# Performance work log

Hardware: AMD Instinct MI355X
Metric: run time of the kernel (lower is better)

The kernel has to match this reference:

```python
import jax, jax.numpy as jnp
import numpy as np

N = 50000   # nodes
E = 400000  # edges
G = 256     # graphs in batch
D = 256     # out_dim (scalar channel width)
VD = 16     # vector channel width after v_emb


def setup_inputs() -> dict:
    key = jax.random.key(0)
    ks = jax.random.split(key, 12)

    def rn(k, shape, scale=0.02):
        return (jax.random.normal(k, shape) * scale).astype(jnp.float32)

    return dict(
        node_s=jax.random.normal(ks[0], (N, 23), jnp.float32),
        node_v=jax.random.normal(ks[1], (N, 4, 3), jnp.float32),
        edge_s=jax.random.normal(ks[2], (E, 17), jnp.float32),
        edge_index=jax.random.randint(ks[3], (2, E), 0, N, jnp.int32),
        batch=jnp.sort(jax.random.randint(ks[4], (N,), 0, G, jnp.int32)),
        Ws=rn(ks[5], (23, D)), bs=jnp.zeros((D,), jnp.float32),
        Wv=rn(ks[6], (4, VD)), bv=jnp.zeros((VD,), jnp.float32),
        We=rn(ks[7], (18, D)), be=jnp.zeros((D,), jnp.float32),
        Wm1=rn(ks[8], (2 * D + VD + D, D)), bm1=jnp.zeros((D,), jnp.float32),
        Wm2=rn(ks[9], (D, D)), bm2=jnp.zeros((D,), jnp.float32),
        Wn=rn(ks[10], (D + VD, D)), bn=jnp.zeros((D,), jnp.float32),
        gamma=jnp.ones((D,), jnp.float32), beta=jnp.zeros((D,), jnp.float32),
    )


def reference(node_s, node_v, edge_s, edge_index, batch,
              Ws, bs, Wv, bv, We, be, Wm1, bm1, Wm2, bm2, Wn, bn, gamma, beta):
    # --- embeddings ---
    s = node_s @ Ws + bs                                            # [N, D]
    e_in = jnp.concatenate([edge_s, jnp.zeros((edge_s.shape[0], 1), edge_s.dtype)], axis=-1)  # no edge_v branch
    e = e_in @ We + be                                              # [E, D]
    # v_emb: Linear over the 4 vector channels -> [N, VD, 3]
    v = jnp.einsum('nkc,ko->noc', node_v, Wv) + bv[None, :, None]
    v_norm = jnp.linalg.norm(v, axis=-1)                            # [N, VD]

    # --- SimpleGVPConv: gather -> 2-layer MLP per edge -> scatter-mean ---
    src, dst = edge_index[0], edge_index[1]                         # PyG: s_j = s[src], s_i = s[dst]
    m_in = jnp.concatenate([s[dst], s[src], v_norm[src], e], axis=-1)  # [E, 2D+VD+D]
    m = jax.nn.relu(m_in @ Wm1 + bm1) @ Wm2 + bm2                   # [E, D]
    agg = jax.ops.segment_sum(m, dst, num_segments=N)               # [N, D]
    cnt = jax.ops.segment_sum(jnp.ones((E,), m.dtype), dst, num_segments=N)
    s = s + agg / jnp.maximum(cnt, 1.0)[:, None]                    # mean aggr + residual update

    # --- node MLP: Linear -> LayerNorm -> ReLU (dropout = eval identity) ---
    feat = jnp.concatenate([s, v_norm], axis=-1)                    # [N, D+VD]
    h = feat @ Wn + bn                                              # [N, D]
    mu = h.mean(axis=-1, keepdims=True)
    var = h.var(axis=-1, keepdims=True)
    h = (h - mu) * jax.lax.rsqrt(var + 1e-5) * gamma + beta
    h = jax.nn.relu(h)

    # --- global mean pool ---
    gsum = jax.ops.segment_sum(h, batch, num_segments=G)            # [G, D]
    gcnt = jax.ops.segment_sum(jnp.ones((h.shape[0],), h.dtype), batch, num_segments=G)
    return gsum / jnp.maximum(gcnt, 1.0)[:, None]
```

## Files before the change

### kernel.cpp

```cpp
#include <hip/hip_runtime.h>
#include <hip/hip_bf16.h>

typedef unsigned short u16;
typedef __attribute__((ext_vector_type(8))) short short8;
typedef __attribute__((ext_vector_type(4))) short short4v;
typedef __attribute__((ext_vector_type(4))) float f32x4;

#define NN 50000
#define EE 400000
#define GG 256
#define MP 50048
#define KS 64
#define K2 320
#define EWS 260

static __device__ __forceinline__ __hip_bfloat16 f2b(float x) { return __float2bfloat16(x); }
static __device__ __forceinline__ float u16tof(u16 v) {
    unsigned x = ((unsigned)v) << 16;
    float f;
    __builtin_memcpy(&f, &x, 4);
    return f;
}
static __device__ __forceinline__ u16 ftou16(float x) {
    __hip_bfloat16 h = __float2bfloat16(x);
    u16 b;
    __builtin_memcpy(&b, &h, 2);
    return b;
}

static __device__ __forceinline__ float dot256(const float* __restrict__ a,
                                               const float* __restrict__ b, int c) {
    const float* __restrict__ bp = b + c;
    float s0 = 0.f, s1 = 0.f, s2 = 0.f, s3 = 0.f;
    float s4 = 0.f, s5 = 0.f, s6 = 0.f, s7 = 0.f;
#pragma unroll 4
    for (int j = 0; j < 256; j += 8) {
        s0 += a[j]     * bp[(size_t)(j)     * 256];
        s1 += a[j + 1] * bp[(size_t)(j + 1) * 256];
        s2 += a[j + 2] * bp[(size_t)(j + 2) * 256];
        s3 += a[j + 3] * bp[(size_t)(j + 3) * 256];
        s4 += a[j + 4] * bp[(size_t)(j + 4) * 256];
        s5 += a[j + 5] * bp[(size_t)(j + 5) * 256];
        s6 += a[j + 6] * bp[(size_t)(j + 6) * 256];
        s7 += a[j + 7] * bp[(size_t)(j + 7) * 256];
    }
    return ((s0 + s1) + (s2 + s3)) + ((s4 + s5) + (s6 + s7));
}

__global__ __launch_bounds__(256) void phase1(const float* __restrict__ Wm1,
                                              const float* __restrict__ Wn,
                                              const float* __restrict__ Wm2,
                                              const float* __restrict__ We,
                                              const float* __restrict__ be,
                                              const float* __restrict__ bm1,
                                              const float* __restrict__ bm2,
                                              const float* __restrict__ Ws,
                                              const float* __restrict__ bs,
                                              __hip_bfloat16* __restrict__ W1pqT,
                                              __hip_bfloat16* __restrict__ W2T,
                                              float* __restrict__ Wc, float* __restrict__ bc,
                                              float* __restrict__ crow,
                                              const float* __restrict__ node_s,
                                              const float* __restrict__ node_v,
                                              const float* __restrict__ Wv,
                                              const float* __restrict__ bv,
                                              __hip_bfloat16* __restrict__ XL2,
                                              const int* __restrict__ ei,
                                              const int* __restrict__ batch,
                                              int* __restrict__ cnt,
                                              int* __restrict__ gstart) {
    int blk = blockIdx.x, tid = threadIdx.x;
    if (blk < 64) {
        int k = blk;
#pragma unroll
        for (int half = 0; half < 2; ++half) {
            int c = half * 256 + tid;
            int cc = c & 255;
            const float* Wm1h = (c < 256) ? Wm1 : (Wm1 + 256 * 256);
            float v = 0.f;
            if (k < 23) v = dot256(&Ws[k * 256], Wm1h, cc);
            else if (k < 39) { if (c >= 256) v = Wm1[(512 + (k - 23)) * 256 + cc]; }
            else if (k == 39) v = dot256(bs, Wm1h, cc);
            W1pqT[c * KS + k] = f2b(v);
        }
    } else if (blk < 384) {
        int k = blk - 64, c = tid;
        float v = 0.f;
        if (k < 23) v = dot256(&Ws[k * 256], Wn, c);
        else if (k < 39) v = Wn[(256 + (k - 23)) * 256 + c];
        else if (k == 39) v = dot256(bs, Wn, c);
        else if (k < 296) v = dot256(&Wm2[(k - 40) * 256], Wn, c);
        W2T[c * K2 + k] = f2b(v);
    } else if (blk < 403) {
        int b = blk - 384, c = tid;
        if (b < 17) Wc[b * 256 + c] = dot256(&We[b * 256], &Wm1[528 * 256], c);
        else if (b == 17) bc[c] = bm1[c] + dot256(be, &Wm1[528 * 256], c);
        else crow[c] = dot256(bm2, Wn, c);
    } else if (blk < 12903) {
        int w = tid >> 6, lane = tid & 63;
        int n = (blk - 403) * 4 + w;
        if (n < NN) {
            float lv = (lane < 23) ? node_s[(size_t)n * 23 + lane] : 0.f;
            float vv = (lane < 12) ? node_v[(size_t)n * 12 + lane] : 0.f;
            float nvk[12];
#pragma unroll
            for (int k = 0; k < 12; ++k) nvk[k] = __shfl(vv, k, 64);
            float vn = 0.f;
            if (lane < 16) {
                float b0 = bv[lane];
                float vx = b0, vy = b0, vz = b0;
#pragma unroll
                for (int k = 0; k < 4; ++k) {
                    float wv = Wv[k * 16 + lane];
                    vx += nvk[k * 3 + 0] * wv;
                    vy += nvk[k * 3 + 1] * wv;
                    vz += nvk[k * 3 + 2] * wv;
                }
                vn = sqrtf(vx * vx + vy * vy + vz * vz);
            }
            int vsrc = (lane >= 23 && lane < 39) ? (lane - 23) : 0;
            float vbc = __shfl(vn, vsrc, 64);
            float outv;
            if (lane < 23) outv = lv;
            else if (lane < 39) outv = vbc;
            else if (lane == 39) outv = 1.f;
            else outv = 0.f;
            __hip_bfloat16* row = XL2 + (size_t)n * K2;
            row[lane] = f2b(outv);
            if (lane < 24) row[296 + lane] = f2b(0.f);
        }
    } else if (blk < 14466) {
        int e = (blk - 12903) * 256 + tid;
        if (e < EE) atomicAdd(&cnt[ei[EE + e]], 1);
    } else {
        int n = (blk - 14466) * 256 + tid;
        if (n < NN) {
            int bn = batch[n];
            int bp = (n == 0) ? -1 : batch[n - 1];
            for (int g = bp + 1; g <= bn; ++g) gstart[g] = n;
            if (n == NN - 1)
                for (int g = bn + 1; g <= GG; ++g) gstart[g] = NN;
        }
    }
}

__global__ __launch_bounds__(256) void scan1(const int* __restrict__ cnt, int* __restrict__ rowptr,
                                             int* __restrict__ bsum) {
    int tid = threadIdx.x, i = blockIdx.x * 256 + tid;
    __shared__ int sd[256];
    int v = (i < NN) ? cnt[i] : 0;
    sd[tid] = v;
    __syncthreads();
    for (int off = 1; off < 256; off <<= 1) {
        int t = (tid >= off) ? sd[tid - off] : 0;
        __syncthreads();
        sd[tid] += t;
        __syncthreads();
    }
    if (i < NN) rowptr[i] = sd[tid] - v;
    if (tid == 255) bsum[blockIdx.x] = sd[255];
}
__global__ __launch_bounds__(256) void scan2(int* __restrict__ bsum, const int* __restrict__ gstart,
                                             float* __restrict__ ginv) {
    int c = threadIdx.x;
    __shared__ int sd[256];
    int v = (c < 196) ? bsum[c] : 0;
    sd[c] = v;
    __syncthreads();
    for (int off = 1; off < 256; off <<= 1) {
        int t = (c >= off) ? sd[c - off] : 0;
        __syncthreads();
        sd[c] += t;
        __syncthreads();
    }
    if (c < 196) bsum[c] = sd[c] - v;
    ginv[c] = 1.f / fmaxf((float)(gstart[c + 1] - gstart[c]), 1.f);
}
__global__ __launch_bounds__(256) void scan3(const int* __restrict__ cnt, const int* __restrict__ bsum,
                                             int* __restrict__ rowptr, int* __restrict__ cursor) {
    int i = blockIdx.x * 256 + threadIdx.x;
    if (i < NN) {
        int v = rowptr[i] + bsum[blockIdx.x];
        rowptr[i] = v;
        cursor[i] = v;
        if (i == NN - 1) rowptr[NN] = v + cnt[i];
    }
}

__global__ __launch_bounds__(256, 2) void gemm1_fill(const u16* __restrict__ A, const u16* __restrict__ Bt,
                                                     __hip_bfloat16* __restrict__ C,
                                                     const int* __restrict__ ei, int* __restrict__ cursor,
                                                     int* __restrict__ eid,
                                                     const float* __restrict__ Wc,
                                                     u16* __restrict__ WcBf) {
    __shared__ __align__(16) u16 At[128 * 64];
    __shared__ __align__(16) u16 Bs[128 * 64];
    int blk = blockIdx.x, tid = threadIdx.x;
    if (blk >= 1564) {
        if (blk == 3127) {
            for (int idx = tid; idx < 8192; idx += 256) {
                int ni = idx >> 9;
                int l = (idx >> 3) & 63;
                int j = idx & 7;
                int k = ((l >> 4) << 3) + j;
                int c = ni * 16 + (l & 15);
                float v = (k < 17) ? Wc[k * 256 + c] : 0.f;
                WcBf[idx] = ftou16(v);
            }
            return;
        }
        int e = (blk - 1564) * 256 + tid;
        if (e < EE) {
            int d = ei[EE + e];
            int pos = atomicAdd(&cursor[d], 1);
            eid[pos] = e;
        }
        return;
    }
    long m0 = (long)(blk >> 2) * 128;
    long n0 = (long)(blk & 3) * 128;
    int wid = tid >> 6, lane = tid & 63;
    int wm = wid >> 1, wn = wid & 1;
    int quad = lane >> 4, l16 = lane & 15;
    f32x4 acc[4][4] = {};
    int r0 = tid >> 3;
    int cc = (tid & 7) * 8;
    const u16* Ab = A + (m0 + r0) * K2 + cc;
    const u16* Bb = Bt + (n0 + r0) * KS + cc;
#pragma unroll
    for (int i = 0; i < 4; ++i) {
        int row = r0 + i * 32;
        __builtin_amdgcn_global_load_lds(
            (const __attribute__((address_space(1))) void*)(Ab + (long)(i * 32) * K2),
            (__attribute__((address_space(3))) void*)(&At[row * 64 + cc]), 16, 0, 0);
    }
#pragma unroll
    for (int i = 0; i < 4; ++i) {
        int row = r0 + i * 32;
        __builtin_amdgcn_global_load_lds(
            (const __attribute__((address_space(1))) void*)(Bb + (long)(i * 32) * KS),
            (__attribute__((address_space(3))) void*)(&Bs[row * 64 + cc]), 16, 0, 0);
    }
    __syncthreads();
#pragma unroll
    for (int kk = 0; kk < 64; kk += 32) {
        short8 af[4], bf[4];
#pragma unroll
        for (int mi = 0; mi < 4; ++mi)
            af[mi] = *(const short8*)&At[(wm * 64 + mi * 16 + l16) * 64 + kk + quad * 8];
#pragma unroll
        for (int ni = 0; ni < 4; ++ni)
            bf[ni] = *(const short8*)&Bs[(wn * 64 + ni * 16 + l16) * 64 + kk + quad * 8];
#pragma unroll
        for (int mi = 0; mi < 4; ++mi) {
#pragma unroll
            for (int ni = 0; ni < 4; ++ni)
                acc[mi][ni] = __builtin_amdgcn_mfma_f32_16x16x32_bf16(af[mi], bf[ni], acc[mi][ni], 0, 0, 0);
        }
    }
#pragma unroll
    for (int mi = 0; mi < 4; ++mi) {
#pragma unroll
        for (int ni = 0; ni < 4; ++ni) {
            long row = m0 + wm * 64 + mi * 16 + quad * 4;
            long col = n0 + wn * 64 + ni * 16 + l16;
#pragma unroll
            for (int r = 0; r < 4; ++r)
                C[(row + r) * 512 + col] = f2b(acc[mi][ni][r]);
        }
    }
}

__global__ __launch_bounds__(64, 1) void edge_agg(const u16* __restrict__ PQ,
                                                  const float* __restrict__ edge_s,
                                                  const int* __restrict__ ei, const int* __restrict__ eid,
                                                  const int* __restrict__ rowptr,
                                                  const u16* __restrict__ WcBf,
                                                  const float* __restrict__ bc, __hip_bfloat16* __restrict__ XL2) {
    __shared__ __align__(16) u16 EW[16 * EWS];
    int lane = threadIdx.x;
    int n = blockIdx.x;
    int start = rowptr[n], deg = rowptr[n + 1] - start;
    int l16 = lane & 15, quad = lane >> 4;
    short8 wcf[16];
#pragma unroll
    for (int ni = 0; ni < 16; ++ni)
        wcf[ni] = *(const short8*)&WcBf[ni * 512 + lane * 8];
    f32x4 bc4 = *(const f32x4*)&bc[lane * 4];
    short4v p4 = *(const short4v*)&PQ[(size_t)n * 512 + lane * 4];
    f32x4 pb;
#pragma unroll
    for (int i = 0; i < 4; ++i) pb[i] = u16tof((u16)p4[i]) + bc4[i];
    f32x4 acc = {0.f, 0.f, 0.f, 0.f};
    const f32x4 zf = {0.f, 0.f, 0.f, 0.f};
    for (int base = 0; base < deg; base += 64) {
        int m = deg - base;
        if (m > 64) m = 64;
        int ee = 0, ss = 0;
        if (lane < m) {
            ee = eid[start + base + lane];
            ss = ei[ee];
        }
        int s0 = __builtin_amdgcn_readlane(ss, 0);
        short4v q0 = *(const short4v*)&PQ[(size_t)s0 * 512 + 256 + lane * 4];
        int ng = (m + 15) >> 4;
        for (int g = 0; g < ng; ++g) {
            int ev = __shfl(ee, g * 16 + l16, 64);
            const float* ep = edge_s + (size_t)ev * 17 + quad * 8;
            float a0 = 0.f, a1 = 0.f, a2 = 0.f, a3 = 0.f, a4 = 0.f, a5 = 0.f, a6 = 0.f, a7 = 0.f;
            if (quad < 2) {
                a0 = ep[0]; a1 = ep[1]; a2 = ep[2]; a3 = ep[3];
                a4 = ep[4]; a5 = ep[5]; a6 = ep[6]; a7 = ep[7];
            } else if (quad == 2) {
                a0 = ep[0];
            }
            short8 af;
            af[0] = (short)ftou16(a0); af[1] = (short)ftou16(a1);
            af[2] = (short)ftou16(a2); af[3] = (short)ftou16(a3);
            af[4] = (short)ftou16(a4); af[5] = (short)ftou16(a5);
            af[6] = (short)ftou16(a6); af[7] = (short)ftou16(a7);
#pragma unroll
            for (int ni = 0; ni < 16; ++ni) {
                f32x4 ew = __builtin_amdgcn_mfma_f32_16x16x32_bf16(af, wcf[ni], zf, 0, 0, 0);
#pragma unroll
                for (int r = 0; r < 4; ++r)
                    EW[(quad * 4 + r) * EWS + ni * 16 + l16] = ftou16(ew[r]);
            }
            int mg = m - g * 16;
            if (mg > 16) mg = 16;
            for (int jj = 0; jj < mg; ++jj) {
                int ja = g * 16 + jj;
                short4v q1 = q0;
                if (ja + 1 < m) {
                    int s1 = __builtin_amdgcn_readlane(ss, ja + 1);
                    q1 = *(const short4v*)&PQ[(size_t)s1 * 512 + 256 + lane * 4];
                }
                short4v ew4 = *(const short4v*)&EW[jj * EWS + lane * 4];
#pragma unroll
                for (int i = 0; i < 4; ++i)
                    acc[i] += fmaxf(pb[i] + u16tof((u16)q0[i]) + u16tof((u16)ew4[i]), 0.f);
                q0 = q1;
            }
        }
    }
    float inv = 1.f / fmaxf((float)deg, 1.f);
    short4v ov;
#pragma unroll
    for (int i = 0; i < 4; ++i) ov[i] = (short)ftou16(acc[i] * inv);
    *(short4v*)&XL2[(size_t)n * K2 + 40 + lane * 4] = ov;
}

__global__ __launch_bounds__(256, 2) void gemm2_lnp(const u16* __restrict__ A, const u16* __restrict__ Bt,
                                                    const int* __restrict__ cnt, const int* __restrict__ batch,
                                                    const float* __restrict__ bn, const float* __restrict__ crow,
                                                    const float* __restrict__ gamma, const float* __restrict__ beta,
                                                    const float* __restrict__ ginv, float* __restrict__ out) {
    __shared__ __align__(16) u16 At[64 * 64];
    __shared__ __align__(16) u16 Bs[256 * 64];
    __shared__ float rsum[4][64], rsum2[4][64];
    __shared__ int sdeg[64], sbatch[64];
    int tid = threadIdx.x;
    long m0 = (long)blockIdx.x * 64;
    int w = tid >> 6, lane = tid & 63;
    int quad = lane >> 4, l16 = lane & 15;
    f32x4 acc[4][4] = {};
    int r0 = tid >> 3;
    int cc = (tid & 7) * 8;
    const u16* Ab = A + (m0 + r0) * K2 + cc;
    const u16* Bb = Bt + (long)r0 * K2 + cc;
    for (int kt = 0; kt < K2; kt += 64) {
#pragma unroll
        for (int i = 0; i < 2; ++i) {
            int row = r0 + i * 32;
            __builtin_amdgcn_global_load_lds(
                (const __attribute__((address_space(1))) void*)(Ab + (long)(i * 32) * K2 + kt),
                (__attribute__((address_space(3))) void*)(&At[row * 64 + cc]), 16, 0, 0);
        }
#pragma unroll
        for (int i = 0; i < 8; ++i) {
            int row = r0 + i * 32;
            __builtin_amdgcn_global_load_lds(
                (const __attribute__((address_space(1))) void*)(Bb + (long)(i * 32) * K2 + kt),
                (__attribute__((address_space(3))) void*)(&Bs[row * 64 + cc]), 16, 0, 0);
        }
        __syncthreads();
#pragma unroll
        for (int kk = 0; kk < 64; kk += 32) {
            short8 af[4], bf[4];
#pragma unroll
            for (int mi = 0; mi < 4; ++mi)
                af[mi] = *(const short8*)&At[(mi * 16 + l16) * 64 + kk + quad * 8];
#pragma unroll
            for (int ni = 0; ni < 4; ++ni)
                bf[ni] = *(const short8*)&Bs[(w * 64 + ni * 16 + l16) * 64 + kk + quad * 8];
#pragma unroll
            for (int mi = 0; mi < 4; ++mi) {
#pragma unroll
                for (int ni = 0; ni < 4; ++ni)
                    acc[mi][ni] = __builtin_amdgcn_mfma_f32_16x16x32_bf16(af[mi], bf[ni], acc[mi][ni], 0, 0, 0);
            }
        }
        __syncthreads();
    }
    if (tid < 64) {
        long n = m0 + tid;
        sdeg[tid] = (n < NN) ? cnt[n] : 0;
        sbatch[tid] = (n < NN) ? batch[n] : -1;
    }
    __syncthreads();
    float bn_l[4], cr_l[4], g_l[4], be_l[4];
#pragma unroll
    for (int ni = 0; ni < 4; ++ni) {
        int col = w * 64 + ni * 16 + l16;
        bn_l[ni] = bn[col];
        cr_l[ni] = crow[col];
        g_l[ni] = gamma[col];
        be_l[ni] = beta[col];
    }
#pragma unroll
    for (int mi = 0; mi < 4; ++mi) {
#pragma unroll
        for (int r = 0; r < 4; ++r) {
            int row = mi * 16 + quad * 4 + r;
            float cr_on = (sdeg[row] > 0) ? 1.f : 0.f;
            float s = 0.f, s2 = 0.f;
#pragma unroll
            for (int ni = 0; ni < 4; ++ni) {
                float xv = acc[mi][ni][r] + bn_l[ni] + cr_on * cr_l[ni];
                acc[mi][ni][r] = xv;
                s += xv;
                s2 += xv * xv;
            }
            s += __shfl_xor(s, 1, 64);  s2 += __shfl_xor(s2, 1, 64);
            s += __shfl_xor(s, 2, 64);  s2 += __shfl_xor(s2, 2, 64);
            s += __shfl_xor(s, 4, 64);  s2 += __shfl_xor(s2, 4, 64);
            s += __shfl_xor(s, 8, 64);  s2 += __shfl_xor(s2, 8, 64);
            if (l16 == 0) { rsum[w][row] = s; rsum2[w][row] = s2; }
        }
    }
    __syncthreads();
    float mu_a[4][4], rs_a[4][4];
#pragma unroll
    for (int mi = 0; mi < 4; ++mi) {
#pragma unroll
        for (int r = 0; r < 4; ++r) {
            int row = mi * 16 + quad * 4 + r;
            float S = rsum[0][row] + rsum[1][row] + rsum[2][row] + rsum[3][row];
            float S2 = rsum2[0][row] + rsum2[1][row] + rsum2[2][row] + rsum2[3][row];
            float mu = S * (1.f / 256.f);
            mu_a[mi][r] = mu;
            rs_a[mi][r] = rsqrtf(S2 * (1.f / 256.f) - mu * mu + 1e-5f);
        }
    }
#pragma unroll
    for (int ni = 0; ni < 4; ++ni) {
        int col = w * 64 + ni * 16 + l16;
        float pacc = 0.f;
        int curg = -1;
#pragma unroll
        for (int mi = 0; mi < 4; ++mi) {
#pragma unroll
            for (int r = 0; r < 4; ++r) {
                int row = mi * 16 + quad * 4 + r;
                int g = sbatch[row];
                float y = (acc[mi][ni][r] - mu_a[mi][r]) * rs_a[mi][r] * g_l[ni] + be_l[ni];
                y = fmaxf(y, 0.f);
                if (g != curg) {
                    if (curg >= 0) atomicAdd(&out[curg * 256 + col], pacc * ginv[curg]);
                    pacc = 0.f;
                    curg = g;
                }
                if (g >= 0) pacc += y;
            }
        }
        if (curg >= 0) atomicAdd(&out[curg * 256 + col], pacc * ginv[curg]);
    }
}

extern "C" void kernel_launch(void* const* d_in, const int* in_sizes, int n_in,
                              void* d_out, int out_size, void* d_ws, size_t ws_size,
                              hipStream_t stream) {
    const float* node_s = (const float*)d_in[0];
    const float* node_v = (const float*)d_in[1];
    const float* edge_s = (const float*)d_in[2];
    const int* ei = (const int*)d_in[3];
    const int* batch = (const int*)d_in[4];
    const float* Ws = (const float*)d_in[5];
    const float* bs = (const float*)d_in[6];
    const float* Wv = (const float*)d_in[7];
    const float* bv = (const float*)d_in[8];
    const float* We = (const float*)d_in[9];
    const float* be = (const float*)d_in[10];
    const float* Wm1 = (const float*)d_in[11];
    const float* bm1 = (const float*)d_in[12];
    const float* Wm2 = (const float*)d_in[13];
    const float* bm2 = (const float*)d_in[14];
    const float* Wn = (const float*)d_in[15];
    const float* bn = (const float*)d_in[16];
    const float* gamma = (const float*)d_in[17];
    const float* beta = (const float*)d_in[18];

    char* ws = (char*)d_ws;
    size_t off = 0;
    auto take = [&](size_t n) {
        void* p = ws + off;
        off = (off + n + 255) & ~(size_t)255;
        return p;
    };
    __hip_bfloat16* XL2 = (__hip_bfloat16*)take((size_t)MP * K2 * 2);
    __hip_bfloat16* PQ = (__hip_bfloat16*)take((size_t)MP * 512 * 2);
    __hip_bfloat16* W1pqT = (__hip_bfloat16*)take(512 * KS * 2);
    __hip_bfloat16* W2T = (__hip_bfloat16*)take(256 * K2 * 2);
    float* Wc = (float*)take(17 * 256 * 4);
    float* bc = (float*)take(256 * 4);
    float* crow = (float*)take(256 * 4);
    u16* WcBf = (u16*)take(16 * 512 * 2);
    int* cnt = (int*)take(NN * 4);
    int* gstart = (int*)take((GG + 1) * 4);
    float* ginv = (float*)take(GG * 4);
    int* rowptr = (int*)take((NN + 1) * 4);
    int* cursor = (int*)take(NN * 4);
    int* eid = (int*)take(EE * 4);
    int* bsum = (int*)take(256 * 4);

    hipMemsetAsync(cnt, 0, NN * 4, stream);
    hipMemsetAsync(d_out, 0, (size_t)out_size * 4, stream);

    phase1<<<14662, 256, 0, stream>>>(Wm1, Wn, Wm2, We, be, bm1, bm2, Ws, bs,
                                      W1pqT, W2T, Wc, bc, crow,
                                      node_s, node_v, Wv, bv, XL2, ei, batch, cnt, gstart);

    scan1<<<196, 256, 0, stream>>>(cnt, rowptr, bsum);
    scan2<<<1, 256, 0, stream>>>(bsum, gstart, ginv);
    scan3<<<196, 256, 0, stream>>>(cnt, bsum, rowptr, cursor);

    gemm1_fill<<<3128, 256, 0, stream>>>((const u16*)XL2, (const u16*)W1pqT, PQ, ei, cursor, eid,
                                         Wc, WcBf);

    edge_agg<<<NN, 64, 0, stream>>>((const u16*)PQ, edge_s, ei, eid, rowptr, WcBf, bc, XL2);

    gemm2_lnp<<<782, 256, 0, stream>>>((const u16*)XL2, (const u16*)W2T, cnt, batch,
                                       bn, crow, gamma, beta, ginv, (float*)d_out);
}
```

Measured before the change: 311.9 us.

## Pre-pack edge features into MFMA layout and batch neighbor loads in edge_agg

Adds an es_pack kernel that gathers edge_s rows in CSR order, converts them to bf16 and stores them in MFMA A-fragment layout per 16-edge group. edge_agg then reads these packed fragments with prefetch, processes globally aligned 16-edge groups, issues all 16 neighbor PQ loads up front, and packs two nodes per 128-thread block. The aim is to raise memory-level parallelism and cut the dependent-load latency of the serial gather. In exchange it adds a kernel launch and an extra packed buffer write and read, and boundary groups shared by adjacent nodes run the MFMA redundantly.

Result: slower. 394.1 us (+26.4%).

```diff
diff --git a/kernel.cpp b/kernel.cpp
--- a/kernel.cpp
+++ b/kernel.cpp
@@ -13,6 +13,7 @@
 #define KS 64
 #define K2 320
 #define EWS 260
+#define NG (EE / 16)
 
 static __device__ __forceinline__ __hip_bfloat16 f2b(float x) { return __float2bfloat16(x); }
 static __device__ __forceinline__ float u16tof(u16 v) {
@@ -271,16 +272,47 @@
     }
 }
 
-__global__ __launch_bounds__(64, 1) void edge_agg(const u16* __restrict__ PQ,
-                                                  const float* __restrict__ edge_s,
-                                                  const int* __restrict__ ei, const int* __restrict__ eid,
-                                                  const int* __restrict__ rowptr,
-                                                  const u16* __restrict__ WcBf,
-                                                  const float* __restrict__ bc, __hip_bfloat16* __restrict__ XL2) {
-    __shared__ __align__(16) u16 EW[16 * EWS];
-    int lane = threadIdx.x;
-    int n = blockIdx.x;
-    int start = rowptr[n], deg = rowptr[n + 1] - start;
+__global__ __launch_bounds__(256) void es_pack(const float* __restrict__ edge_s,
+                                               const int* __restrict__ eid,
+                                               u16* __restrict__ esP) {
+    int tid = threadIdx.x;
+    int wv = tid >> 6, lane = tid & 63;
+    int G = blockIdx.x * 4 + wv;
+    int l16 = lane & 15, quad = lane >> 4;
+    if (quad == 3) return;
+    int p = G * 16 + l16;
+    int ev = eid[p];
+    const float* ep = edge_s + (size_t)ev * 17 + quad * 8;
+    float a0 = 0.f, a1 = 0.f, a2 = 0.f, a3 = 0.f, a4 = 0.f, a5 = 0.f, a6 = 0.f, a7 = 0.f;
+    if (quad < 2) {
+        a0 = ep[0]; a1 = ep[1]; a2 = ep[2]; a3 = ep[3];
+        a4 = ep[4]; a5 = ep[5]; a6 = ep[6]; a7 = ep[7];
+    } else {
+        a0 = ep[0];
+    }
+    short8 af;
+    af[0] = (short)ftou16(a0); af[1] = (short)ftou16(a1);
+    af[2] = (short)ftou16(a2); af[3] = (short)ftou16(a3);
+    af[4] = (short)ftou16(a4); af[5] = (short)ftou16(a5);
+    af[6] = (short)ftou16(a6); af[7] = (short)ftou16(a7);
+    *(short8*)&esP[(size_t)G * 384 + lane * 8] = af;
+}
+
+__global__ __launch_bounds__(128, 4) void edge_agg(const u16* __restrict__ PQ,
+                                                   const u16* __restrict__ esP,
+                                                   const int* __restrict__ ei, const int* __restrict__ eid,
+                                                   const int* __restrict__ rowptr,
+                                                   const u16* __restrict__ WcBf,
+                                                   const float* __restrict__ bc,
+                                                   __hip_bfloat16* __restrict__ XL2) {
+    __shared__ __align__(16) u16 EWall[2][16 * EWS];
+    int tid = threadIdx.x;
+    int wv = tid >> 6, lane = tid & 63;
+    int n = blockIdx.x * 2 + wv;
+    if (n >= NN) return;
+    u16* __restrict__ EW = &EWall[wv][0];
+    int start = rowptr[n], end = rowptr[n + 1];
+    int deg = end - start;
     int l16 = lane & 15, quad = lane >> 4;
     short8 wcf[16];
 #pragma unroll
@@ -293,53 +325,73 @@
     for (int i = 0; i < 4; ++i) pb[i] = u16tof((u16)p4[i]) + bc4[i];
     f32x4 acc = {0.f, 0.f, 0.f, 0.f};
     const f32x4 zf = {0.f, 0.f, 0.f, 0.f};
-    for (int base = 0; base < deg; base += 64) {
-        int m = deg - base;
-        if (m > 64) m = 64;
-        int ee = 0, ss = 0;
-        if (lane < m) {
-            ee = eid[start + base + lane];
-            ss = ei[ee];
-        }
-        int s0 = __builtin_amdgcn_readlane(ss, 0);
-        short4v q0 = *(const short4v*)&PQ[(size_t)s0 * 512 + 256 + lane * 4];
-        int ng = (m + 15) >> 4;
-        for (int g = 0; g < ng; ++g) {
-            int ev = __shfl(ee, g * 16 + l16, 64);
-            const float* ep = edge_s + (size_t)ev * 17 + quad * 8;
-            float a0 = 0.f, a1 = 0.f, a2 = 0.f, a3 = 0.f, a4 = 0.f, a5 = 0.f, a6 = 0.f, a7 = 0.f;
-            if (quad < 2) {
-                a0 = ep[0]; a1 = ep[1]; a2 = ep[2]; a3 = ep[3];
-                a4 = ep[4]; a5 = ep[5]; a6 = ep[6]; a7 = ep[7];
-            } else if (quad == 2) {
-                a0 = ep[0];
-            }
-            short8 af;
-            af[0] = (short)ftou16(a0); af[1] = (short)ftou16(a1);
-            af[2] = (short)ftou16(a2); af[3] = (short)ftou16(a3);
-            af[4] = (short)ftou16(a4); af[5] = (short)ftou16(a5);
-            af[6] = (short)ftou16(a6); af[7] = (short)ftou16(a7);
-#pragma unroll
-            for (int ni = 0; ni < 16; ++ni) {
-                f32x4 ew = __builtin_amdgcn_mfma_f32_16x16x32_bf16(af, wcf[ni], zf, 0, 0, 0);
-#pragma unroll
-                for (int r = 0; r < 4; ++r)
-                    EW[(quad * 4 + r) * EWS + ni * 16 + l16] = ftou16(ew[r]);
-            }
-            int mg = m - g * 16;
-            if (mg > 16) mg = 16;
-            for (int jj = 0; jj < mg; ++jj) {
-                int ja = g * 16 + jj;
-                short4v q1 = q0;
-                if (ja + 1 < m) {
-                    int s1 = __builtin_amdgcn_readlane(ss, ja + 1);
-                    q1 = *(const short4v*)&PQ[(size_t)s1 * 512 + 256 + lane * 4];
+    if (deg > 0) {
+        int G0 = start >> 4;
+        int G1 = (end - 1) >> 4;
+        short8 afc = {};
+        if (quad < 3) afc = *(const short8*)&esP[(size_t)G0 * 384 + lane * 8];
+        for (int Gb = G0; Gb <= G1; Gb += 4) {
+            int base = Gb << 4;
+            int p = base + lane;
+            int ss = 0;
+            if (p < EE) ss = ei[eid[p]];
+            int lo = start - base; if (lo < 0) lo = 0;
+            int le = end - base;   if (le > 64) le = 64;
+            int lem1 = le - 1;
+            int Ge = Gb + 3; if (Ge > G1) Ge = G1;
+            for (int G = Gb; G <= Ge; ++G) {
+                int gb = (G - Gb) << 4;
+                int cl = lo > gb ? lo : gb;
+                int ch = (gb + 16 < le) ? gb + 16 : le;
+                auto loadQ = [&](int pl) {
+                    int pc = pl < cl ? cl : (pl > lem1 ? lem1 : pl);
+                    int s = __builtin_amdgcn_readlane(ss, pc);
+                    return *(const short4v*)&PQ[(size_t)s * 512 + 256 + lane * 4];
+                };
+                short4v q0 = loadQ(gb + 0),  q1 = loadQ(gb + 1);
+                short4v q2 = loadQ(gb + 2),  q3 = loadQ(gb + 3);
+                short4v q4 = loadQ(gb + 4),  q5 = loadQ(gb + 5);
+                short4v q6 = loadQ(gb + 6),  q7 = loadQ(gb + 7);
+                short4v q8 = loadQ(gb + 8),  q9 = loadQ(gb + 9);
+                short4v q10 = loadQ(gb + 10), q11 = loadQ(gb + 11);
+                short4v q12 = loadQ(gb + 12), q13 = loadQ(gb + 13);
+                short4v q14 = loadQ(gb + 14), q15 = loadQ(gb + 15);
+                short8 af = afc;
+                int Gn = G + 1; if (Gn > G1) Gn = G1;
+                if (quad < 3) afc = *(const short8*)&esP[(size_t)Gn * 384 + lane * 8];
+#pragma unroll
+                for (int ni = 0; ni < 16; ++ni) {
+                    f32x4 ew = __builtin_amdgcn_mfma_f32_16x16x32_bf16(af, wcf[ni], zf, 0, 0, 0);
+#pragma unroll
+                    for (int r = 0; r < 4; ++r)
+                        EW[(quad * 4 + r) * EWS + ni * 16 + l16] = ftou16(ew[r]);
                 }
-                short4v ew4 = *(const short4v*)&EW[jj * EWS + lane * 4];
-#pragma unroll
-                for (int i = 0; i < 4; ++i)
-                    acc[i] += fmaxf(pb[i] + u16tof((u16)q0[i]) + u16tof((u16)ew4[i]), 0.f);
-                q0 = q1;
+#define CONSUME_U(QQ, c)                                                            \
+                {                                                                   \
+                    short4v ew4 = *(const short4v*)&EW[(c) * EWS + lane * 4];       \
+                    _Pragma("unroll")                                               \
+                    for (int i = 0; i < 4; ++i)                                     \
+                        acc[i] += fmaxf(pb[i] + u16tof((u16)QQ[i]) +                \
+                                        u16tof((u16)ew4[i]), 0.f);                  \
+                }
+#define CONSUME_G(QQ, c)                                                            \
+                {                                                                   \
+                    int pl = gb + (c);                                              \
+                    if (pl >= cl && pl < ch) CONSUME_U(QQ, c)                       \
+                }
+                if (cl == gb && ch == gb + 16) {
+                    CONSUME_U(q0, 0)  CONSUME_U(q1, 1)  CONSUME_U(q2, 2)  CONSUME_U(q3, 3)
+                    CONSUME_U(q4, 4)  CONSUME_U(q5, 5)  CONSUME_U(q6, 6)  CONSUME_U(q7, 7)
+                    CONSUME_U(q8, 8)  CONSUME_U(q9, 9)  CONSUME_U(q10, 10) CONSUME_U(q11, 11)
+                    CONSUME_U(q12, 12) CONSUME_U(q13, 13) CONSUME_U(q14, 14) CONSUME_U(q15, 15)
+                } else {
+                    CONSUME_G(q0, 0)  CONSUME_G(q1, 1)  CONSUME_G(q2, 2)  CONSUME_G(q3, 3)
+                    CONSUME_G(q4, 4)  CONSUME_G(q5, 5)  CONSUME_G(q6, 6)  CONSUME_G(q7, 7)
+                    CONSUME_G(q8, 8)  CONSUME_G(q9, 9)  CONSUME_G(q10, 10) CONSUME_G(q11, 11)
+                    CONSUME_G(q12, 12) CONSUME_G(q13, 13) CONSUME_G(q14, 14) CONSUME_G(q15, 15)
+                }
+#undef CONSUME_U
+#undef CONSUME_G
             }
         }
     }
@@ -515,6 +567,7 @@
     float* bc = (float*)take(256 * 4);
     float* crow = (float*)take(256 * 4);
     u16* WcBf = (u16*)take(16 * 512 * 2);
+    u16* esP = (u16*)take((size_t)NG * 384 * 2);
     int* cnt = (int*)take(NN * 4);
     int* gstart = (int*)take((GG + 1) * 4);
     float* ginv = (float*)take(GG * 4);
@@ -537,7 +590,9 @@
     gemm1_fill<<<3128, 256, 0, stream>>>((const u16*)XL2, (const u16*)W1pqT, PQ, ei, cursor, eid,
                                          Wc, WcBf);
 
-    edge_agg<<<NN, 64, 0, stream>>>((const u16*)PQ, edge_s, ei, eid, rowptr, WcBf, bc, XL2);
+    es_pack<<<NG / 4, 256, 0, stream>>>(edge_s, eid, esP);
+
+    edge_agg<<<25000, 128, 0, stream>>>((const u16*)PQ, esP, ei, eid, rowptr, WcBf, bc, XL2);
 
     gemm2_lnp<<<782, 256, 0, stream>>>((const u16*)XL2, (const u16*)W2T, cnt, batch,
                                        bn, crow, gamma, beta, ginv, (float*)d_out);
```

## Parallelize edge aggregation over fixed 16-edge groups with atomic fp32 accumulation

Applied to the files above, without the earlier changes.

Replaces the one-wave-per-node edge aggregation, which is load-imbalanced by node degree, with fixed 16-edge groups taken from the dst-sorted edge order. Each wave processes exactly 16 edges and flushes partial sums per destination into an fp32 buffer using atomics. A new finalize kernel divides by degree and writes bf16 into XL2. The fp32 buffer is zeroed inside phase1. This adds a 51MB accumulation buffer, extra atomic traffic and one more kernel launch, and it loses the per-node register-resident P row reuse.

Result: slower. 501.7 us (+60.9%).

```diff
diff --git a/kernel.cpp b/kernel.cpp
--- a/kernel.cpp
+++ b/kernel.cpp
@@ -13,6 +13,8 @@
 #define KS 64
 #define K2 320
 #define EWS 260
+#define NG (EE / 16)
+#define ZB 12500
 
 static __device__ __forceinline__ __hip_bfloat16 f2b(float x) { return __float2bfloat16(x); }
 static __device__ __forceinline__ float u16tof(u16 v) {
@@ -68,7 +70,8 @@
                                               const int* __restrict__ ei,
                                               const int* __restrict__ batch,
                                               int* __restrict__ cnt,
-                                              int* __restrict__ gstart) {
+                                              int* __restrict__ gstart,
+                                              float* __restrict__ XL2acc) {
     int blk = blockIdx.x, tid = threadIdx.x;
     if (blk < 64) {
         int k = blk;
@@ -132,7 +135,7 @@
     } else if (blk < 14466) {
         int e = (blk - 12903) * 256 + tid;
         if (e < EE) atomicAdd(&cnt[ei[EE + e]], 1);
-    } else {
+    } else if (blk < 14662) {
         int n = (blk - 14466) * 256 + tid;
         if (n < NN) {
             int bn = batch[n];
@@ -141,6 +144,10 @@
             if (n == NN - 1)
                 for (int g = bn + 1; g <= GG; ++g) gstart[g] = NN;
         }
+    } else {
+        size_t idx = ((size_t)(blk - 14662) * 256 + tid) * 4;
+        f32x4 z = {0.f, 0.f, 0.f, 0.f};
+        *(f32x4*)&XL2acc[idx] = z;
     }
 }
 
@@ -271,83 +278,103 @@
     }
 }
 
-__global__ __launch_bounds__(64, 1) void edge_agg(const u16* __restrict__ PQ,
-                                                  const float* __restrict__ edge_s,
-                                                  const int* __restrict__ ei, const int* __restrict__ eid,
-                                                  const int* __restrict__ rowptr,
-                                                  const u16* __restrict__ WcBf,
-                                                  const float* __restrict__ bc, __hip_bfloat16* __restrict__ XL2) {
-    __shared__ __align__(16) u16 EW[16 * EWS];
-    int lane = threadIdx.x;
-    int n = blockIdx.x;
-    int start = rowptr[n], deg = rowptr[n + 1] - start;
+__global__ __launch_bounds__(256) void edge_agg(const u16* __restrict__ PQ,
+                                                const float* __restrict__ edge_s,
+                                                const int* __restrict__ ei,
+                                                const int* __restrict__ eid,
+                                                const u16* __restrict__ WcBf,
+                                                const float* __restrict__ bc,
+                                                float* __restrict__ XL2acc) {
+    __shared__ __align__(16) u16 EWall[4][16 * EWS];
+    int tid = threadIdx.x;
+    int wv = tid >> 6, lane = tid & 63;
+    int G = blockIdx.x * 4 + wv;
+    u16* __restrict__ EW = &EWall[wv][0];
     int l16 = lane & 15, quad = lane >> 4;
-    short8 wcf[16];
-#pragma unroll
-    for (int ni = 0; ni < 16; ++ni)
-        wcf[ni] = *(const short8*)&WcBf[ni * 512 + lane * 8];
+    int e = 0, ssrc = 0, sdst = 0;
+    if (lane < 16) {
+        e = eid[G * 16 + lane];
+        ssrc = ei[e];
+        sdst = ei[EE + e];
+    }
+    int ev = __shfl(e, l16, 64);
+    const float* ep = edge_s + (size_t)ev * 17 + quad * 8;
+    float a0 = 0.f, a1 = 0.f, a2 = 0.f, a3 = 0.f, a4 = 0.f, a5 = 0.f, a6 = 0.f, a7 = 0.f;
+    if (quad < 2) {
+        a0 = ep[0]; a1 = ep[1]; a2 = ep[2]; a3 = ep[3];
+        a4 = ep[4]; a5 = ep[5]; a6 = ep[6]; a7 = ep[7];
+    } else if (quad == 2) {
+        a0 = ep[0];
+    }
     f32x4 bc4 = *(const f32x4*)&bc[lane * 4];
-    short4v p4 = *(const short4v*)&PQ[(size_t)n * 512 + lane * 4];
-    f32x4 pb;
-#pragma unroll
-    for (int i = 0; i < 4; ++i) pb[i] = u16tof((u16)p4[i]) + bc4[i];
-    f32x4 acc = {0.f, 0.f, 0.f, 0.f};
+#define LQ(jj) (*(const short4v*)&PQ[(size_t)__builtin_amdgcn_readlane(ssrc, (jj)) * 512 + 256 + lane * 4])
+#define LP(jj) (*(const short4v*)&PQ[(size_t)__builtin_amdgcn_readlane(sdst, (jj)) * 512 + lane * 4])
+    short4v qa0 = LQ(0), qa1 = LQ(1), qa2 = LQ(2), qa3 = LQ(3);
+    short4v qa4 = LQ(4), qa5 = LQ(5), qa6 = LQ(6), qa7 = LQ(7);
+    short4v pa0 = LP(0), pa1 = LP(1), pa2 = LP(2), pa3 = LP(3);
+    short4v pa4 = LP(4), pa5 = LP(5), pa6 = LP(6), pa7 = LP(7);
+    short8 af;
+    af[0] = (short)ftou16(a0); af[1] = (short)ftou16(a1);
+    af[2] = (short)ftou16(a2); af[3] = (short)ftou16(a3);
+    af[4] = (short)ftou16(a4); af[5] = (short)ftou16(a5);
+    af[6] = (short)ftou16(a6); af[7] = (short)ftou16(a7);
     const f32x4 zf = {0.f, 0.f, 0.f, 0.f};
-    for (int base = 0; base < deg; base += 64) {
-        int m = deg - base;
-        if (m > 64) m = 64;
-        int ee = 0, ss = 0;
-        if (lane < m) {
-            ee = eid[start + base + lane];
-            ss = ei[ee];
-        }
-        int s0 = __builtin_amdgcn_readlane(ss, 0);
-        short4v q0 = *(const short4v*)&PQ[(size_t)s0 * 512 + 256 + lane * 4];
-        int ng = (m + 15) >> 4;
-        for (int g = 0; g < ng; ++g) {
-            int ev = __shfl(ee, g * 16 + l16, 64);
-            const float* ep = edge_s + (size_t)ev * 17 + quad * 8;
-            float a0 = 0.f, a1 = 0.f, a2 = 0.f, a3 = 0.f, a4 = 0.f, a5 = 0.f, a6 = 0.f, a7 = 0.f;
-            if (quad < 2) {
-                a0 = ep[0]; a1 = ep[1]; a2 = ep[2]; a3 = ep[3];
-                a4 = ep[4]; a5 = ep[5]; a6 = ep[6]; a7 = ep[7];
-            } else if (quad == 2) {
-                a0 = ep[0];
-            }
-            short8 af;
-            af[0] = (short)ftou16(a0); af[1] = (short)ftou16(a1);
-            af[2] = (short)ftou16(a2); af[3] = (short)ftou16(a3);
-            af[4] = (short)ftou16(a4); af[5] = (short)ftou16(a5);
-            af[6] = (short)ftou16(a6); af[7] = (short)ftou16(a7);
-#pragma unroll
-            for (int ni = 0; ni < 16; ++ni) {
-                f32x4 ew = __builtin_amdgcn_mfma_f32_16x16x32_bf16(af, wcf[ni], zf, 0, 0, 0);
-#pragma unroll
-                for (int r = 0; r < 4; ++r)
-                    EW[(quad * 4 + r) * EWS + ni * 16 + l16] = ftou16(ew[r]);
-            }
-            int mg = m - g * 16;
-            if (mg > 16) mg = 16;
-            for (int jj = 0; jj < mg; ++jj) {
-                int ja = g * 16 + jj;
-                short4v q1 = q0;
-                if (ja + 1 < m) {
-                    int s1 = __builtin_amdgcn_readlane(ss, ja + 1);
-                    q1 = *(const short4v*)&PQ[(size_t)s1 * 512 + 256 + lane * 4];
-                }
-                short4v ew4 = *(const short4v*)&EW[jj * EWS + lane * 4];
-#pragma unroll
-                for (int i = 0; i < 4; ++i)
-                    acc[i] += fmaxf(pb[i] + u16tof((u16)q0[i]) + u16tof((u16)ew4[i]), 0.f);
-                q0 = q1;
-            }
-        }
-    }
-    float inv = 1.f / fmaxf((float)deg, 1.f);
-    short4v ov;
-#pragma unroll
-    for (int i = 0; i < 4; ++i) ov[i] = (short)ftou16(acc[i] * inv);
-    *(short4v*)&XL2[(size_t)n * K2 + 40 + lane * 4] = ov;
+#pragma unroll
+    for (int ni = 0; ni < 16; ++ni) {
+        short8 wf = *(const short8*)&WcBf[ni * 512 + lane * 8];
+        f32x4 ew = __builtin_amdgcn_mfma_f32_16x16x32_bf16(af, wf, zf, 0, 0, 0);
+#pragma unroll
+        for (int r = 0; r < 4; ++r)
+            EW[(quad * 4 + r) * EWS + ni * 16 + l16] = ftou16(ew[r]);
+    }
+    short4v qb0 = LQ(8),  qb1 = LQ(9),  qb2 = LQ(10), qb3 = LQ(11);
+    short4v qb4 = LQ(12), qb5 = LQ(13), qb6 = LQ(14), qb7 = LQ(15);
+    short4v pb0 = LP(8),  pb1 = LP(9),  pb2 = LP(10), pb3 = LP(11);
+    short4v pb4 = LP(12), pb5 = LP(13), pb6 = LP(14), pb7 = LP(15);
+#undef LQ
+#undef LP
+    f32x4 racc = {0.f, 0.f, 0.f, 0.f};
+    int dcur = __builtin_amdgcn_readlane(sdst, 0);
+#define FLUSH                                                                       \
+    {                                                                               \
+        float* fp = XL2acc + (size_t)dcur * 256 + lane * 4;                         \
+        atomicAdd(fp + 0, racc[0]); atomicAdd(fp + 1, racc[1]);                     \
+        atomicAdd(fp + 2, racc[2]); atomicAdd(fp + 3, racc[3]);                     \
+        racc[0] = 0.f; racc[1] = 0.f; racc[2] = 0.f; racc[3] = 0.f;                 \
+    }
+#define CONSUME(PP, QQ, c)                                                          \
+    {                                                                               \
+        int d_ = __builtin_amdgcn_readlane(sdst, (c));                              \
+        if (d_ != dcur) { FLUSH; dcur = d_; }                                       \
+        short4v ew4 = *(const short4v*)&EW[(c) * EWS + lane * 4];                   \
+        _Pragma("unroll")                                                           \
+        for (int i = 0; i < 4; ++i)                                                 \
+            racc[i] += fmaxf(u16tof((u16)PP[i]) + bc4[i] + u16tof((u16)QQ[i]) +     \
+                             u16tof((u16)ew4[i]), 0.f);                             \
+    }
+    CONSUME(pa0, qa0, 0)  CONSUME(pa1, qa1, 1)  CONSUME(pa2, qa2, 2)  CONSUME(pa3, qa3, 3)
+    CONSUME(pa4, qa4, 4)  CONSUME(pa5, qa5, 5)  CONSUME(pa6, qa6, 6)  CONSUME(pa7, qa7, 7)
+    CONSUME(pb0, qb0, 8)  CONSUME(pb1, qb1, 9)  CONSUME(pb2, qb2, 10) CONSUME(pb3, qb3, 11)
+    CONSUME(pb4, qb4, 12) CONSUME(pb5, qb5, 13) CONSUME(pb6, qb6, 14) CONSUME(pb7, qb7, 15)
+    FLUSH
+#undef CONSUME
+#undef FLUSH
+}
+
+__global__ __launch_bounds__(256) void fin(const float* __restrict__ XL2acc,
+                                           const int* __restrict__ cnt,
+                                           __hip_bfloat16* __restrict__ XL2) {
+    int tid = threadIdx.x;
+    int n = blockIdx.x * 4 + (tid >> 6);
+    int lane = tid & 63;
+    if (n < NN) {
+        f32x4 a = *(const f32x4*)&XL2acc[(size_t)n * 256 + lane * 4];
+        float inv = 1.f / fmaxf((float)cnt[n], 1.f);
+        short4v ov;
+#pragma unroll
+        for (int i = 0; i < 4; ++i) ov[i] = (short)ftou16(a[i] * inv);
+        *(short4v*)&XL2[(size_t)n * K2 + 40 + lane * 4] = ov;
+    }
 }
 
 __global__ __launch_bounds__(256, 2) void gemm2_lnp(const u16* __restrict__ A, const u16* __restrict__ Bt,
@@ -458,7 +485,7 @@
         float pacc = 0.f;
         int curg = -1;
 #pragma unroll
-        for (int mi = 0; mi < 4; ++mi) {
+    for (int mi = 0; mi < 4; ++mi) {
 #pragma unroll
             for (int r = 0; r < 4; ++r) {
                 int row = mi * 16 + quad * 4 + r;
@@ -515,6 +542,7 @@
     float* bc = (float*)take(256 * 4);
     float* crow = (float*)take(256 * 4);
     u16* WcBf = (u16*)take(16 * 512 * 2);
+    float* XL2acc = (float*)take((size_t)NN * 256 * 4);
     int* cnt = (int*)take(NN * 4);
     int* gstart = (int*)take((GG + 1) * 4);
     float* ginv = (float*)take(GG * 4);
@@ -526,9 +554,10 @@
     hipMemsetAsync(cnt, 0, NN * 4, stream);
     hipMemsetAsync(d_out, 0, (size_t)out_size * 4, stream);
 
-    phase1<<<14662, 256, 0, stream>>>(Wm1, Wn, Wm2, We, be, bm1, bm2, Ws, bs,
-                                      W1pqT, W2T, Wc, bc, crow,
-                                      node_s, node_v, Wv, bv, XL2, ei, batch, cnt, gstart);
+    phase1<<<14662 + ZB, 256, 0, stream>>>(Wm1, Wn, Wm2, We, be, bm1, bm2, Ws, bs,
+                                           W1pqT, W2T, Wc, bc, crow,
+                                           node_s, node_v, Wv, bv, XL2, ei, batch, cnt, gstart,
+                                           XL2acc);
 
     scan1<<<196, 256, 0, stream>>>(cnt, rowptr, bsum);
     scan2<<<1, 256, 0, stream>>>(bsum, gstart, ginv);
@@ -537,7 +566,9 @@
     gemm1_fill<<<3128, 256, 0, stream>>>((const u16*)XL2, (const u16*)W1pqT, PQ, ei, cursor, eid,
                                          Wc, WcBf);
 
-    edge_agg<<<NN, 64, 0, stream>>>((const u16*)PQ, edge_s, ei, eid, rowptr, WcBf, bc, XL2);
+    edge_agg<<<NG / 4, 256, 0, stream>>>((const u16*)PQ, edge_s, ei, eid, WcBf, bc, XL2acc);
+
+    fin<<<12500, 256, 0, stream>>>(XL2acc, cnt, XL2);
 
     gemm2_lnp<<<782, 256, 0, stream>>>((const u16*)XL2, (const u16*)W2T, cnt, batch,
                                        bn, crow, gamma, beta, ginv, (float*)d_out);
```
